# Optimization experiments

Hardware: AMD Instinct MI355X
Metric: run time of the kernel (lower is better)

The kernel has to match this reference:

```python
import jax, jax.numpy as jnp
import numpy as np

B, T, C = 4, 2048, 1024
H = 16
DH = C // H  # 64


def setup_inputs() -> dict:
    key = jax.random.key(0)
    ks = jax.random.split(key, 10)
    s_in = 1.0 / np.sqrt(C)
    x = jax.random.normal(ks[0], (B, T, C), dtype=jnp.float32)
    # stacked per-head projection weights: [H, C, DH]
    Wq = jax.random.normal(ks[1], (H, C, DH), dtype=jnp.float32) * s_in
    bq = jnp.zeros((H, DH), dtype=jnp.float32)
    Wk = jax.random.normal(ks[2], (H, C, DH), dtype=jnp.float32) * s_in
    bk = jnp.zeros((H, DH), dtype=jnp.float32)
    Wv = jax.random.normal(ks[3], (H, C, DH), dtype=jnp.float32) * s_in
    bv = jnp.zeros((H, DH), dtype=jnp.float32)
    Wo = jax.random.normal(ks[4], (C, C), dtype=jnp.float32) * s_in
    bo = jnp.zeros((C,), dtype=jnp.float32)
    return {"x": x, "Wq": Wq, "bq": bq, "Wk": Wk, "bk": bk,
            "Wv": Wv, "bv": bv, "Wo": Wo, "bo": bo}


def reference(x, Wq, bq, Wk, bk, Wv, bv, Wo, bo):
    # per-head projections: (B,T,C) x (H,C,DH) -> (B,H,T,DH)
    q = jnp.einsum('btc,hcd->bhtd', x, Wq) + bq[None, :, None, :]
    k = jnp.einsum('btc,hcd->bhtd', x, Wk) + bk[None, :, None, :]
    v = jnp.einsum('btc,hcd->bhtd', x, Wv) + bv[None, :, None, :]
    # scores scaled by C**-0.5 (C = full input embedding dim, as in source)
    scale = jnp.float32(C) ** -0.5
    scores = jnp.einsum('bhtd,bhsd->bhts', q, k) * scale  # (B,H,T,T)
    causal = jnp.tril(jnp.ones((T, T), dtype=bool))
    scores = jnp.where(causal, scores, -jnp.inf)
    attn = jax.nn.softmax(scores, axis=-1)
    out = jnp.einsum('bhts,bhsd->bhtd', attn, v)  # (B,H,T,DH)
    out = out.transpose(0, 2, 1, 3).reshape(B, T, C)  # concat heads
    return out @ Wo + bo
```

## Files before the change

### kernel.cpp

```cpp
#include <hip/hip_runtime.h>
#include <hip/hip_bf16.h>

#define TDIM 2048
#define BDIM 4
#define CDIM 1024
#define HDIM 16
#define DH   64

typedef __hip_bfloat16 bf16;
typedef __attribute__((ext_vector_type(8))) short bf16x8;
typedef __attribute__((ext_vector_type(4))) short bf16x4;
typedef __attribute__((ext_vector_type(4))) float f32x4;

__device__ __forceinline__ void async_ld16(const bf16* g, bf16* l) {
    __builtin_amdgcn_global_load_lds(
        (const __attribute__((address_space(1))) unsigned int*)g,
        (__attribute__((address_space(3))) unsigned int*)l, 16, 0, 0);
}

__device__ __forceinline__ unsigned short bf16bits(float x) {
    bf16 b = __float2bfloat16(x);
    return *(unsigned short*)&b;
}

__device__ __forceinline__ f32x4 mfma_16x16x16_bf16(bf16x4 a, bf16x4 b, f32x4 c) {
#if __has_builtin(__builtin_amdgcn_mfma_f32_16x16x16_bf16)
    return __builtin_amdgcn_mfma_f32_16x16x16_bf16(a, b, c, 0, 0, 0);
#elif __has_builtin(__builtin_amdgcn_mfma_f32_16x16x16bf16_1k)
    return __builtin_amdgcn_mfma_f32_16x16x16bf16_1k(a, b, c, 0, 0, 0);
#else
    asm volatile("v_mfma_f32_16x16x16_bf16 %0, %1, %2, %0"
                 : "+v"(c) : "v"(a), "v"(b));
    return c;
#endif
}

__global__ void convert_x4(const float4* __restrict__ src, ushort4* __restrict__ dst, int n4) {
    int i = blockIdx.x * blockDim.x + threadIdx.x;
    if (i >= n4) return;
    float4 v = src[i];
    ushort4 o;
    o.x = bf16bits(v.x); o.y = bf16bits(v.y);
    o.z = bf16bits(v.z); o.w = bf16bits(v.w);
    dst[i] = o;
}

__global__ void convert_biases(const float* __restrict__ b0, const float* __restrict__ b1,
                               const float* __restrict__ b2, const float* __restrict__ b3,
                               bf16* __restrict__ dst) {
    int i = blockIdx.x * blockDim.x + threadIdx.x;
    int which = i >> 10, j = i & 1023;
    const float* src = (which == 0) ? b0 : (which == 1) ? b1 : (which == 2) ? b2 : b3;
    dst[i] = __float2bfloat16(src[j]);
}

__global__ __launch_bounds__(256) void transpose_qkv_kernel(
    const float* __restrict__ Wq, const float* __restrict__ Wk, const float* __restrict__ Wv,
    bf16* __restrict__ WqT, bf16* __restrict__ WkT, bf16* __restrict__ WvT) {
    __shared__ float tile[64][65];
    const int which = blockIdx.z >> 4, h = blockIdx.z & 15;
    const float* W  = ((which == 0) ? Wq  : (which == 1) ? Wk  : Wv)  + (size_t)h * CDIM * DH;
    bf16*        WT = ((which == 0) ? WqT : (which == 1) ? WkT : WvT) + (size_t)h * CDIM * DH;
    const int c0 = blockIdx.x * 64;
    for (int it = 0; it < 16; it++) {
        int e = it * 256 + threadIdx.x;
        int r = e >> 6, col = e & 63;
        tile[r][col] = W[(size_t)(c0 + r) * DH + col];
    }
    __syncthreads();
    for (int it = 0; it < 16; it++) {
        int e = it * 256 + threadIdx.x;
        int r = e >> 6, col = e & 63;
        WT[(size_t)r * CDIM + c0 + col] = __float2bfloat16(tile[col][r]);
    }
}

__global__ __launch_bounds__(256) void transpose_wo_kernel(
    const float* __restrict__ W, bf16* __restrict__ WT) {
    __shared__ float tile[64][65];
    const int c0 = blockIdx.x * 64, d0 = blockIdx.y * 64;
    for (int it = 0; it < 16; it++) {
        int e = it * 256 + threadIdx.x;
        int r = e >> 6, col = e & 63;
        tile[r][col] = W[(size_t)(c0 + r) * CDIM + d0 + col];
    }
    __syncthreads();
    for (int it = 0; it < 16; it++) {
        int e = it * 256 + threadIdx.x;
        int r = e >> 6, col = e & 63;
        WT[(size_t)(d0 + r) * CDIM + c0 + col] = __float2bfloat16(tile[col][r]);
    }
}

__global__ __launch_bounds__(256) void transpose_v_kernel(
    const bf16* __restrict__ V, bf16* __restrict__ Vt) {
    __shared__ unsigned short tile[64][65];
    const int bh = blockIdx.y, t0 = blockIdx.x * 64;
    const unsigned short* Vp  = (const unsigned short*)V + ((size_t)bh * TDIM + t0) * DH;
    unsigned short*       Vtp = (unsigned short*)Vt + (size_t)bh * DH * TDIM;
    for (int it = 0; it < 16; it++) {
        int e = it * 256 + threadIdx.x;
        int r = e >> 6, c = e & 63;
        tile[r][c] = Vp[(size_t)r * DH + c];
    }
    __syncthreads();
    for (int it = 0; it < 16; it++) {
        int e = it * 256 + threadIdx.x;
        int r = e >> 6, c = e & 63;
        Vtp[(size_t)r * TDIM + t0 + c] = tile[c][r];
    }
}

__global__ __launch_bounds__(256) void proj_qkv_kernel(
    const bf16* __restrict__ X,
    const bf16* __restrict__ WqT, const bf16* __restrict__ WkT, const bf16* __restrict__ WvT,
    const bf16* __restrict__ bq,  const bf16* __restrict__ bk,  const bf16* __restrict__ bvv,
    bf16* __restrict__ Qo, bf16* __restrict__ Ko, bf16* __restrict__ Vo)
{
    const int z = blockIdx.z;
    const bf16* Bt   = (z == 0) ? WqT : (z == 1) ? WkT : WvT;
    const bf16* bias = (z == 0) ? bq  : (z == 1) ? bk  : bvv;

    __shared__ __align__(16) bf16 As[128 * 32];
    __shared__ __align__(16) bf16 Bs[128 * 32];

    const int tid  = threadIdx.x;
    const int lane = tid & 63;
    const int wave = tid >> 6;
    const int wr = wave >> 1, wc = wave & 1;
    const int l15 = lane & 15, quad = lane >> 4;

    const int blockM = blockIdx.y * 128;
    const int blockN = blockIdx.x * 128;

    f32x4 acc[4][4];
    for (int i = 0; i < 4; i++)
        for (int j = 0; j < 4; j++)
            acc[i][j] = (f32x4){0.f, 0.f, 0.f, 0.f};

    const int srow = lane >> 2, scol = (lane & 3) * 8;
    for (int k0 = 0; k0 < CDIM; k0 += 32) {
        for (int cc = 0; cc < 2; cc++) {
            int chunk = wave * 2 + cc;
            int row = chunk * 16 + srow;
            async_ld16(&X [(size_t)(blockM + row) * CDIM + k0 + scol], &As[chunk * 512]);
            async_ld16(&Bt[(size_t)(blockN + row) * CDIM + k0 + scol], &Bs[chunk * 512]);
        }
        __syncthreads();

        bf16x8 af[4], bfr[4];
        for (int mi = 0; mi < 4; mi++)
            af[mi] = *(const bf16x8*)&As[(wr * 64 + mi * 16 + l15) * 32 + quad * 8];
        for (int ni = 0; ni < 4; ni++)
            bfr[ni] = *(const bf16x8*)&Bs[(wc * 64 + ni * 16 + l15) * 32 + quad * 8];

        for (int mi = 0; mi < 4; mi++)
            for (int ni = 0; ni < 4; ni++)
                acc[mi][ni] = __builtin_amdgcn_mfma_f32_16x16x32_bf16(
                    af[mi], bfr[ni], acc[mi][ni], 0, 0, 0);
        __syncthreads();
    }

    for (int mi = 0; mi < 4; mi++) {
        int mbase = blockM + wr * 64 + mi * 16 + quad * 4;
        for (int ni = 0; ni < 4; ni++) {
            int n = blockN + wc * 64 + ni * 16 + l15;
            float bval = __bfloat162float(bias[n]);
            int h = n >> 6, d = n & 63;
            for (int r = 0; r < 4; r++) {
                int mm = mbase + r;
                int b = mm >> 11, t = mm & 2047;
                float val = acc[mi][ni][r] + bval;
                size_t idx = (((size_t)b * HDIM + h) * TDIM + t) * DH + d;
                if (z == 0)      Qo[idx] = __float2bfloat16(val * 0.03125f);
                else if (z == 1) Ko[idx] = __float2bfloat16(val);
                else             Vo[idx] = __float2bfloat16(val);
            }
        }
    }
}

__global__ __launch_bounds__(256) void proj_out_kernel(
    const bf16* __restrict__ X, const bf16* __restrict__ Bt,
    const bf16* __restrict__ bias, float* __restrict__ Out)
{
    __shared__ __align__(16) bf16 As[128 * 32];
    __shared__ __align__(16) bf16 Bs[128 * 32];

    const int tid  = threadIdx.x;
    const int lane = tid & 63;
    const int wave = tid >> 6;
    const int wr = wave >> 1, wc = wave & 1;
    const int l15 = lane & 15, quad = lane >> 4;

    const int blockM = blockIdx.y * 128;
    const int blockN = blockIdx.x * 128;

    f32x4 acc[4][4];
    for (int i = 0; i < 4; i++)
        for (int j = 0; j < 4; j++)
            acc[i][j] = (f32x4){0.f, 0.f, 0.f, 0.f};

    const int srow = lane >> 2, scol = (lane & 3) * 8;
    for (int k0 = 0; k0 < CDIM; k0 += 32) {
        for (int cc = 0; cc < 2; cc++) {
            int chunk = wave * 2 + cc;
            int row = chunk * 16 + srow;
            async_ld16(&X [(size_t)(blockM + row) * CDIM + k0 + scol], &As[chunk * 512]);
            async_ld16(&Bt[(size_t)(blockN + row) * CDIM + k0 + scol], &Bs[chunk * 512]);
        }
        __syncthreads();

        bf16x8 af[4], bfr[4];
        for (int mi = 0; mi < 4; mi++)
            af[mi] = *(const bf16x8*)&As[(wr * 64 + mi * 16 + l15) * 32 + quad * 8];
        for (int ni = 0; ni < 4; ni++)
            bfr[ni] = *(const bf16x8*)&Bs[(wc * 64 + ni * 16 + l15) * 32 + quad * 8];

        for (int mi = 0; mi < 4; mi++)
            for (int ni = 0; ni < 4; ni++)
                acc[mi][ni] = __builtin_amdgcn_mfma_f32_16x16x32_bf16(
                    af[mi], bfr[ni], acc[mi][ni], 0, 0, 0);
        __syncthreads();
    }

    for (int mi = 0; mi < 4; mi++) {
        int mbase = blockM + wr * 64 + mi * 16 + quad * 4;
        for (int ni = 0; ni < 4; ni++) {
            int n = blockN + wc * 64 + ni * 16 + l15;
            float bval = __bfloat162float(bias[n]);
            for (int r = 0; r < 4; r++)
                Out[(size_t)(mbase + r) * CDIM + n] = acc[mi][ni][r] + bval;
        }
    }
}

__global__ __launch_bounds__(256, 4) void attn_kernel(
    const bf16* __restrict__ Q, const bf16* __restrict__ Kb,
    const bf16* __restrict__ Vt, bf16* __restrict__ Y)
{
    const int bh    = blockIdx.y;
    const int qT    = (int)gridDim.x - 1 - blockIdx.x;
    const int qBase = qT * 128;
    const int tid  = threadIdx.x;
    const int lane = tid & 63, wave = tid >> 6;
    const int l15 = lane & 15, quad = lane >> 4;

    __shared__ __align__(16) bf16 Ks[64 * 72];
    __shared__ __align__(16) bf16 Vs[64 * 72];

    bf16x8 qf[2][2];
    for (int g = 0; g < 2; g++) {
        const size_t qrow = (size_t)bh * TDIM + qBase + g * 64 + wave * 16 + l15;
        qf[g][0] = *(const bf16x8*)&Q[qrow * DH + quad * 8];
        qf[g][1] = *(const bf16x8*)&Q[qrow * DH + 32 + quad * 8];
    }

    f32x4 o[2][4];
    for (int g = 0; g < 2; g++)
        for (int mt = 0; mt < 4; mt++)
            o[g][mt] = (f32x4){0.f, 0.f, 0.f, 0.f};
    float lsum[2] = {0.f, 0.f};

    const int r0 = tid >> 3, kc0 = (tid & 7) * 8;

    const int nkt = 2 * qT + 2;
    uint4 kreg0 = *(const uint4*)&Kb[((size_t)bh * TDIM + r0) * DH + kc0];
    uint4 kreg1 = *(const uint4*)&Kb[((size_t)bh * TDIM + r0 + 32) * DH + kc0];
    uint4 vreg0 = *(const uint4*)&Vt[((size_t)bh * DH + r0) * TDIM + kc0];
    uint4 vreg1 = *(const uint4*)&Vt[((size_t)bh * DH + r0 + 32) * TDIM + kc0];

    for (int kt = 0; kt < nkt; kt++) {
        *(uint4*)&Ks[r0 * 72 + kc0]        = kreg0;
        *(uint4*)&Ks[(r0 + 32) * 72 + kc0] = kreg1;
        *(uint4*)&Vs[r0 * 72 + kc0]        = vreg0;
        *(uint4*)&Vs[(r0 + 32) * 72 + kc0] = vreg1;
        __syncthreads();

        if (kt + 1 < nkt) {
            const int nb = (kt + 1) * 64;
            kreg0 = *(const uint4*)&Kb[((size_t)bh * TDIM + nb + r0) * DH + kc0];
            kreg1 = *(const uint4*)&Kb[((size_t)bh * TDIM + nb + r0 + 32) * DH + kc0];
            vreg0 = *(const uint4*)&Vt[((size_t)bh * DH + r0) * TDIM + nb + kc0];
            vreg1 = *(const uint4*)&Vt[((size_t)bh * DH + r0 + 32) * TDIM + nb + kc0];
        }

        const int dg = kt - 2 * qT;
        for (int nt = 0; nt < 4; nt++) {
            bf16x8 kf0 = *(const bf16x8*)&Ks[(nt * 16 + l15) * 72 + quad * 8];
            bf16x8 kf1 = *(const bf16x8*)&Ks[(nt * 16 + l15) * 72 + 32 + quad * 8];
            bf16x4 vA[4];
            for (int mt = 0; mt < 4; mt++)
                vA[mt] = *(const bf16x4*)&Vs[(mt * 16 + l15) * 72 + nt * 16 + quad * 4];

            for (int g = 0; g < 2; g++) {
                if (dg == 1 && g == 0) continue;
                f32x4 s = (f32x4){0.f, 0.f, 0.f, 0.f};
                s = __builtin_amdgcn_mfma_f32_16x16x32_bf16(kf0, qf[g][0], s, 0, 0, 0);
                s = __builtin_amdgcn_mfma_f32_16x16x32_bf16(kf1, qf[g][1], s, 0, 0, 0);

                const bool diag = (dg == g);
                bf16x4 pb;
                for (int r = 0; r < 4; r++) {
                    float pe = __expf(s[r]);
                    if (diag && (nt * 16 + quad * 4 + r > wave * 16 + l15)) pe = 0.f;
                    lsum[g] += pe;
                    pb[r] = (short)bf16bits(pe);
                }
                for (int mt = 0; mt < 4; mt++)
                    o[g][mt] = mfma_16x16x16_bf16(vA[mt], pb, o[g][mt]);
            }
        }
        __syncthreads();
    }

    const int b = bh >> 4, h = bh & 15;
    for (int g = 0; g < 2; g++) {
        float v = lsum[g];
        v += __shfl_xor(v, 16, 64);
        v += __shfl_xor(v, 32, 64);
        const float inv = 1.0f / v;

        for (int mt = 0; mt < 4; mt++) {
            unsigned short pk[4];
            for (int r = 0; r < 4; r++) pk[r] = bf16bits(o[g][mt][r] * inv);
            *(ushort4*)&Ks[(wave * 16 + l15) * 72 + mt * 16 + quad * 4] = *(ushort4*)pk;
        }
        const int qq = lane >> 2, part = lane & 3;
        const int t = qBase + g * 64 + wave * 16 + qq;
        uint4 c0 = *(const uint4*)&Ks[(wave * 16 + qq) * 72 + part * 16];
        uint4 c1 = *(const uint4*)&Ks[(wave * 16 + qq) * 72 + part * 16 + 8];
        *(uint4*)&Y[((size_t)b * TDIM + t) * CDIM + h * DH + part * 16]     = c0;
        *(uint4*)&Y[((size_t)b * TDIM + t) * CDIM + h * DH + part * 16 + 8] = c1;
    }
}

extern "C" void kernel_launch(void* const* d_in, const int* in_sizes, int n_in,
                              void* d_out, int out_size, void* d_ws, size_t ws_size,
                              hipStream_t stream) {
    (void)in_sizes; (void)n_in; (void)out_size; (void)ws_size;

    char* ws = (char*)d_ws;
    const size_t SZ_BHTD = (size_t)BDIM * HDIM * TDIM * DH * sizeof(bf16);
    const size_t SZ_W    = (size_t)HDIM * CDIM * DH * sizeof(bf16);
    bf16* Qb  = (bf16*)(ws);
    bf16* Kb  = (bf16*)(ws + SZ_BHTD);
    bf16* Vt  = (bf16*)(ws + 2 * SZ_BHTD);
    bf16* Y   = (bf16*)(ws + 3 * SZ_BHTD);
    bf16* WqT = (bf16*)(ws + 4 * SZ_BHTD);
    bf16* WkT = (bf16*)(ws + 4 * SZ_BHTD + SZ_W);
    bf16* WvT = (bf16*)(ws + 4 * SZ_BHTD + 2 * SZ_W);
    bf16* WoT = (bf16*)(ws + 4 * SZ_BHTD + 3 * SZ_W);
    bf16* xC  = (bf16*)(ws + 4 * SZ_BHTD + 4 * SZ_W);
    bf16* bqC = (bf16*)(ws + 5 * SZ_BHTD + 4 * SZ_W);
    bf16* bkC = bqC + 1024;
    bf16* bvC = bqC + 2048;
    bf16* boC = bqC + 3072;
    bf16* Vb  = (bf16*)d_out;

    const int nX4 = (BDIM * TDIM * CDIM) / 4;
    convert_x4<<<nX4 / 256, 256, 0, stream>>>((const float4*)d_in[0], (ushort4*)xC, nX4);
    convert_biases<<<16, 256, 0, stream>>>((const float*)d_in[2], (const float*)d_in[4],
                                           (const float*)d_in[6], (const float*)d_in[8], bqC);

    transpose_qkv_kernel<<<dim3(CDIM / 64, 1, 48), 256, 0, stream>>>(
        (const float*)d_in[1], (const float*)d_in[3], (const float*)d_in[5], WqT, WkT, WvT);
    transpose_wo_kernel<<<dim3(CDIM / 64, CDIM / 64), 256, 0, stream>>>(
        (const float*)d_in[7], WoT);

    dim3 gq(CDIM / 128, (BDIM * TDIM) / 128, 3);
    proj_qkv_kernel<<<gq, 256, 0, stream>>>(xC, WqT, WkT, WvT, bqC, bkC, bvC, Qb, Kb, Vb);

    transpose_v_kernel<<<dim3(TDIM / 64, BDIM * HDIM), 256, 0, stream>>>(Vb, Vt);

    attn_kernel<<<dim3(TDIM / 128, BDIM * HDIM), 256, 0, stream>>>(Qb, Kb, Vt, Y);

    proj_out_kernel<<<dim3(CDIM / 128, (BDIM * TDIM) / 128), 256, 0, stream>>>(
        Y, WoT, boC, (float*)d_out);
}
```

Measured before the change: 300.1 us.

## Split attention query tile across eight waves instead of two groups per wave

The attention block grows from 256 to 512 threads, and each wave now owns 16 query rows instead of two 16-row groups. This halves per-thread register state (one accumulator set, one row sum) and halves the K/V staging loads per thread, with the aim of raising occupancy and latency hiding. Waves in the lower half skip the final diagonal key tile. The cost is more barrier participants per block and some imbalance where half the waves idle on the last tile.

```diff
diff --git a/kernel.cpp b/kernel.cpp
--- a/kernel.cpp
+++ b/kernel.cpp
@@ -235,7 +235,7 @@
     }
 }
 
-__global__ __launch_bounds__(256, 4) void attn_kernel(
+__global__ __launch_bounds__(512, 8) void attn_kernel(
     const bf16* __restrict__ Q, const bf16* __restrict__ Kb,
     const bf16* __restrict__ Vt, bf16* __restrict__ Y)
 {
@@ -246,93 +246,83 @@
     const int lane = tid & 63, wave = tid >> 6;
     const int l15 = lane & 15, quad = lane >> 4;
 
-    __shared__ __align__(16) bf16 Ks[64 * 72];
-    __shared__ __align__(16) bf16 Vs[64 * 72];
-
-    bf16x8 qf[2][2];
-    for (int g = 0; g < 2; g++) {
-        const size_t qrow = (size_t)bh * TDIM + qBase + g * 64 + wave * 16 + l15;
-        qf[g][0] = *(const bf16x8*)&Q[qrow * DH + quad * 8];
-        qf[g][1] = *(const bf16x8*)&Q[qrow * DH + 32 + quad * 8];
-    }
-
-    f32x4 o[2][4];
-    for (int g = 0; g < 2; g++)
-        for (int mt = 0; mt < 4; mt++)
-            o[g][mt] = (f32x4){0.f, 0.f, 0.f, 0.f};
-    float lsum[2] = {0.f, 0.f};
+    __shared__ __align__(16) bf16 smem[128 * 72];
+    bf16* Ks = smem;
+    bf16* Vs = smem + 64 * 72;
+
+    const size_t qrow = (size_t)bh * TDIM + qBase + wave * 16 + l15;
+    const bf16x8 qf0 = *(const bf16x8*)&Q[qrow * DH + quad * 8];
+    const bf16x8 qf1 = *(const bf16x8*)&Q[qrow * DH + 32 + quad * 8];
+
+    f32x4 o[4];
+    for (int mt = 0; mt < 4; mt++) o[mt] = (f32x4){0.f, 0.f, 0.f, 0.f};
+    float lsum = 0.f;
 
     const int r0 = tid >> 3, kc0 = (tid & 7) * 8;
 
-    const int nkt = 2 * qT + 2;
-    uint4 kreg0 = *(const uint4*)&Kb[((size_t)bh * TDIM + r0) * DH + kc0];
-    uint4 kreg1 = *(const uint4*)&Kb[((size_t)bh * TDIM + r0 + 32) * DH + kc0];
-    uint4 vreg0 = *(const uint4*)&Vt[((size_t)bh * DH + r0) * TDIM + kc0];
-    uint4 vreg1 = *(const uint4*)&Vt[((size_t)bh * DH + r0 + 32) * TDIM + kc0];
+    const int nkt   = 2 * qT + 2;
+    const int kdiag = 2 * qT + (wave >> 2);
+    const int qloc  = (wave & 3) * 16 + l15;
+
+    uint4 kreg = *(const uint4*)&Kb[((size_t)bh * TDIM + r0) * DH + kc0];
+    uint4 vreg = *(const uint4*)&Vt[((size_t)bh * DH + r0) * TDIM + kc0];
 
     for (int kt = 0; kt < nkt; kt++) {
-        *(uint4*)&Ks[r0 * 72 + kc0]        = kreg0;
-        *(uint4*)&Ks[(r0 + 32) * 72 + kc0] = kreg1;
-        *(uint4*)&Vs[r0 * 72 + kc0]        = vreg0;
-        *(uint4*)&Vs[(r0 + 32) * 72 + kc0] = vreg1;
+        *(uint4*)&Ks[r0 * 72 + kc0] = kreg;
+        *(uint4*)&Vs[r0 * 72 + kc0] = vreg;
         __syncthreads();
 
         if (kt + 1 < nkt) {
             const int nb = (kt + 1) * 64;
-            kreg0 = *(const uint4*)&Kb[((size_t)bh * TDIM + nb + r0) * DH + kc0];
-            kreg1 = *(const uint4*)&Kb[((size_t)bh * TDIM + nb + r0 + 32) * DH + kc0];
-            vreg0 = *(const uint4*)&Vt[((size_t)bh * DH + r0) * TDIM + nb + kc0];
-            vreg1 = *(const uint4*)&Vt[((size_t)bh * DH + r0 + 32) * TDIM + nb + kc0];
-        }
-
-        const int dg = kt - 2 * qT;
-        for (int nt = 0; nt < 4; nt++) {
-            bf16x8 kf0 = *(const bf16x8*)&Ks[(nt * 16 + l15) * 72 + quad * 8];
-            bf16x8 kf1 = *(const bf16x8*)&Ks[(nt * 16 + l15) * 72 + 32 + quad * 8];
-            bf16x4 vA[4];
-            for (int mt = 0; mt < 4; mt++)
-                vA[mt] = *(const bf16x4*)&Vs[(mt * 16 + l15) * 72 + nt * 16 + quad * 4];
-
-            for (int g = 0; g < 2; g++) {
-                if (dg == 1 && g == 0) continue;
+            kreg = *(const uint4*)&Kb[((size_t)bh * TDIM + nb + r0) * DH + kc0];
+            vreg = *(const uint4*)&Vt[((size_t)bh * DH + r0) * TDIM + nb + kc0];
+        }
+
+        if (kt <= kdiag) {
+            const bool diag = (kt == kdiag);
+            for (int nt = 0; nt < 4; nt++) {
+                bf16x8 kf0 = *(const bf16x8*)&Ks[(nt * 16 + l15) * 72 + quad * 8];
+                bf16x8 kf1 = *(const bf16x8*)&Ks[(nt * 16 + l15) * 72 + 32 + quad * 8];
+                bf16x4 vA[4];
+                for (int mt = 0; mt < 4; mt++)
+                    vA[mt] = *(const bf16x4*)&Vs[(mt * 16 + l15) * 72 + nt * 16 + quad * 4];
+
                 f32x4 s = (f32x4){0.f, 0.f, 0.f, 0.f};
-                s = __builtin_amdgcn_mfma_f32_16x16x32_bf16(kf0, qf[g][0], s, 0, 0, 0);
-                s = __builtin_amdgcn_mfma_f32_16x16x32_bf16(kf1, qf[g][1], s, 0, 0, 0);
-
-                const bool diag = (dg == g);
+                s = __builtin_amdgcn_mfma_f32_16x16x32_bf16(kf0, qf0, s, 0, 0, 0);
+                s = __builtin_amdgcn_mfma_f32_16x16x32_bf16(kf1, qf1, s, 0, 0, 0);
+
                 bf16x4 pb;
                 for (int r = 0; r < 4; r++) {
                     float pe = __expf(s[r]);
-                    if (diag && (nt * 16 + quad * 4 + r > wave * 16 + l15)) pe = 0.f;
-                    lsum[g] += pe;
+                    if (diag && (nt * 16 + quad * 4 + r > qloc)) pe = 0.f;
+                    lsum += pe;
                     pb[r] = (short)bf16bits(pe);
                 }
                 for (int mt = 0; mt < 4; mt++)
-                    o[g][mt] = mfma_16x16x16_bf16(vA[mt], pb, o[g][mt]);
+                    o[mt] = mfma_16x16x16_bf16(vA[mt], pb, o[mt]);
             }
         }
         __syncthreads();
     }
 
+    float v = lsum;
+    v += __shfl_xor(v, 16, 64);
+    v += __shfl_xor(v, 32, 64);
+    const float inv = 1.0f / v;
+
+    unsigned short* sm = (unsigned short*)smem;
+    for (int mt = 0; mt < 4; mt++) {
+        unsigned short pk[4];
+        for (int r = 0; r < 4; r++) pk[r] = bf16bits(o[mt][r] * inv);
+        *(ushort4*)&sm[(wave * 16 + l15) * 72 + mt * 16 + quad * 4] = *(ushort4*)pk;
+    }
     const int b = bh >> 4, h = bh & 15;
-    for (int g = 0; g < 2; g++) {
-        float v = lsum[g];
-        v += __shfl_xor(v, 16, 64);
-        v += __shfl_xor(v, 32, 64);
-        const float inv = 1.0f / v;
-
-        for (int mt = 0; mt < 4; mt++) {
-            unsigned short pk[4];
-            for (int r = 0; r < 4; r++) pk[r] = bf16bits(o[g][mt][r] * inv);
-            *(ushort4*)&Ks[(wave * 16 + l15) * 72 + mt * 16 + quad * 4] = *(ushort4*)pk;
-        }
-        const int qq = lane >> 2, part = lane & 3;
-        const int t = qBase + g * 64 + wave * 16 + qq;
-        uint4 c0 = *(const uint4*)&Ks[(wave * 16 + qq) * 72 + part * 16];
-        uint4 c1 = *(const uint4*)&Ks[(wave * 16 + qq) * 72 + part * 16 + 8];
-        *(uint4*)&Y[((size_t)b * TDIM + t) * CDIM + h * DH + part * 16]     = c0;
-        *(uint4*)&Y[((size_t)b * TDIM + t) * CDIM + h * DH + part * 16 + 8] = c1;
-    }
+    const int qq = lane >> 2, part = lane & 3;
+    const int t = qBase + wave * 16 + qq;
+    uint4 c0 = *(const uint4*)&sm[(wave * 16 + qq) * 72 + part * 16];
+    uint4 c1 = *(const uint4*)&sm[(wave * 16 + qq) * 72 + part * 16 + 8];
+    *(uint4*)&Y[((size_t)b * TDIM + t) * CDIM + h * DH + part * 16]     = c0;
+    *(uint4*)&Y[((size_t)b * TDIM + t) * CDIM + h * DH + part * 16 + 8] = c1;
 }
 
 extern "C" void kernel_launch(void* const* d_in, const int* in_sizes, int n_in,
@@ -373,7 +363,7 @@
 
     transpose_v_kernel<<<dim3(TDIM / 64, BDIM * HDIM), 256, 0, stream>>>(Vb, Vt);
 
-    attn_kernel<<<dim3(TDIM / 128, BDIM * HDIM), 256, 0, stream>>>(Qb, Kb, Vt, Y);
+    attn_kernel<<<dim3(TDIM / 128, BDIM * HDIM), 512, 0, stream>>>(Qb, Kb, Vt, Y);
 
     proj_out_kernel<<<dim3(CDIM / 128, (BDIM * TDIM) / 128), 256, 0, stream>>>(
         Y, WoT, boC, (float*)d_out);
```

Result: slower. 351.6 us (+17.2%).
